# Kernel tuning notes

Measured on AMD Instinct MI355X. Metric: run time of the kernel, lower is better.

The kernel has to match this reference:

```python
import jax, jax.numpy as jnp
import numpy as np

H = 64
VOCAB = 64
SLOTS = 4
N_PASSES = 3
EPS = 1e-5


def _ln(x, g, b):
    m = jnp.mean(x, axis=-1, keepdims=True)
    v = jnp.mean((x - m) ** 2, axis=-1, keepdims=True)
    return (x - m) * jax.lax.rsqrt(v + EPS) * g + b


def setup_inputs() -> dict:
    key = jax.random.key(0)
    ks = iter(jax.random.split(key, 32))
    B, L = 128, 4096
    f = lambda shape, scale=0.05: jax.random.normal(next(ks), shape, dtype=jnp.float32) * scale
    inp = {
        "seq": jax.random.randint(next(ks), (B, L), 0, VOCAB),
        # Encoder
        "embed": f((VOCAB, H), 1.0),
        "ff1_w": f((H, 2 * H)), "ff1_b": jnp.zeros((2 * H,), jnp.float32),
        "ff2_w": f((2 * H, H)), "ff2_b": jnp.zeros((H,), jnp.float32),
        "enc_g": jnp.ones((H,), jnp.float32), "enc_b": jnp.zeros((H,), jnp.float32),
        # ForwardGate
        "g1_w": f((H, H // 2)), "g1_b": jnp.zeros((H // 2,), jnp.float32),
        "g2_w": f((H // 2, 1)), "g2_b": jnp.zeros((1,), jnp.float32),
        # Re-encoding layers (stacked over passes)
        "rq_w": f((N_PASSES, H, H)), "rq_b": jnp.zeros((N_PASSES, H), jnp.float32),
        "rk_w": f((N_PASSES, H, H)), "rk_b": jnp.zeros((N_PASSES, H), jnp.float32),
        "rv_w": f((N_PASSES, H, H)), "rv_b": jnp.zeros((N_PASSES, H), jnp.float32),
        "rn_g": jnp.ones((N_PASSES, H), jnp.float32), "rn_b": jnp.zeros((N_PASSES, H), jnp.float32),
        # ReadHead
        "rd_q_w": f((H, H)), "rd_q_b": jnp.zeros((H,), jnp.float32),
        "out_w": f((H, VOCAB)), "out_b": jnp.zeros((VOCAB,), jnp.float32),
    }
    return inp


def reference(seq, embed, ff1_w, ff1_b, ff2_w, ff2_b, enc_g, enc_b,
              g1_w, g1_b, g2_w, g2_b,
              rq_w, rq_b, rk_w, rk_b, rv_w, rv_b, rn_g, rn_b,
              rd_q_w, rd_q_b, out_w, out_b):
    scale = 1.0 / np.sqrt(H)
    # Encoder: embed + FFN residual + LayerNorm
    h = embed[seq]                                            # (B,L,H)
    ff = jax.nn.relu(h @ ff1_w + ff1_b) @ ff2_w + ff2_b
    hidden = _ln(h + ff, enc_g, enc_b)                        # (B,L,H)
    # Gate scores -> top-k slot selection
    scores = jax.nn.sigmoid(jax.nn.relu(hidden @ g1_w + g1_b) @ g2_w + g2_b)[..., 0]  # (B,L)
    _, idx = jax.lax.top_k(scores, SLOTS)                     # (B,k)
    slots = jnp.take_along_axis(hidden, idx[:, :, None], axis=1)  # (B,k,H)
    # Iterative cross-attention re-encoding
    for p in range(N_PASSES):
        Sq = slots @ rq_w[p] + rq_b[p]                        # (B,k,H)
        Sk = hidden @ rk_w[p] + rk_b[p]                       # (B,L,H)
        Sv = hidden @ rv_w[p] + rv_b[p]
        attn = jax.nn.softmax(jnp.einsum("bkh,blh->bkl", Sq, Sk) * scale, axis=-1)
        slots = _ln(slots + jnp.einsum("bkl,blh->bkh", attn, Sv), rn_g[p], rn_b[p])
    # Read head: attend last-token query over slots
    q = hidden[:, -1, :] @ rd_q_w + rd_q_b                    # (B,H)
    attn = jax.nn.softmax(jnp.einsum("bkh,bh->bk", slots, q) * scale, axis=-1)
    read = jnp.einsum("bk,bkh->bh", attn, slots)
    return read @ out_w + out_b                               # (B,VOCAB)
```

## Files before the change

### kernel.cpp

```cpp
#include <hip/hip_runtime.h>
#include <math.h>

#define H 64
#define VOCAB 64
#define LSEQ 4096
#define NSLOTS 4
#define NP 3
#define EPS 1e-5f

typedef unsigned long long ull;

__device__ __forceinline__ float wsum(float x) {
    #pragma unroll
    for (int m = 1; m < 64; m <<= 1) x += __shfl_xor(x, m);
    return x;
}
__device__ __forceinline__ float wmax(float x) {
    #pragma unroll
    for (int m = 1; m < 64; m <<= 1) x = fmaxf(x, __shfl_xor(x, m));
    return x;
}


__global__ __launch_bounds__(64) void build_all(
    const float* __restrict__ embed,
    const float* __restrict__ ff1_w, const float* __restrict__ ff1_b,
    const float* __restrict__ ff2_w, const float* __restrict__ ff2_b,
    const float* __restrict__ enc_g, const float* __restrict__ enc_b,
    const float* __restrict__ g1_w,  const float* __restrict__ g1_b,
    const float* __restrict__ g2_w,  const float* __restrict__ g2_b,
    const float* __restrict__ rq_w,  const float* __restrict__ rq_b,
    const float* __restrict__ rk_w,  const float* __restrict__ rk_b,
    const float* __restrict__ rv_w,  const float* __restrict__ rv_b,
    const float* __restrict__ rd_q_w, const float* __restrict__ rd_q_b,
    const float* __restrict__ out_w,
    float* __restrict__ enc_t, float* __restrict__ score_t,
    float* __restrict__ c_t, float* __restrict__ q_t,
    float* __restrict__ MT, float* __restrict__ SvT, float* __restrict__ owT)
{
    const int seg  = blockIdx.x >> 6;
    const int v    = blockIdx.x & 63;
    const int lane = threadIdx.x;

    __shared__ float h_s[H];
    __shared__ float a1[2 * H];
    __shared__ float hid_s[H];
    __shared__ float sk_s[H];

    h_s[lane] = embed[v * H + lane];
    __syncthreads();

    float pA[4] = {0, 0, 0, 0}, pB[4] = {0, 0, 0, 0};
    #pragma unroll
    for (int c4 = 0; c4 < 4; c4++)
        #pragma unroll
        for (int d = 0; d < 16; d++) {
            int dd = c4 * 16 + d;
            float hv = h_s[dd];
            pA[c4] += hv * ff1_w[dd * 128 + lane];
            pB[c4] += hv * ff1_w[dd * 128 + lane + 64];
        }
    a1[lane]      = fmaxf(ff1_b[lane]      + ((pA[0] + pA[1]) + (pA[2] + pA[3])), 0.f);
    a1[lane + 64] = fmaxf(ff1_b[lane + 64] + ((pB[0] + pB[1]) + (pB[2] + pB[3])), 0.f);
    __syncthreads();

    float pO[4] = {0, 0, 0, 0};
    #pragma unroll
    for (int c4 = 0; c4 < 4; c4++)
        #pragma unroll
        for (int j = 0; j < 32; j++) {
            int jj = c4 * 32 + j;
            pO[c4] += a1[jj] * ff2_w[jj * H + lane];
        }
    float o = ff2_b[lane] + ((pO[0] + pO[1]) + (pO[2] + pO[3]));

    float x = h_s[lane] + o;
    float s1 = x, s2 = x * x;
    #pragma unroll
    for (int m = 1; m < 64; m <<= 1) { s1 += __shfl_xor(s1, m); s2 += __shfl_xor(s2, m); }
    float mu  = s1 * (1.f / 64.f);
    float var = s2 * (1.f / 64.f) - mu * mu;
    float hid = (x - mu) * rsqrtf(var + EPS) * enc_g[lane] + enc_b[lane];
    hid_s[lane] = hid;
    __syncthreads();

    if (seg == 0) {
        enc_t[v * H + lane] = hid;
        float p = 0.f;
        if (lane < 32) {
            float a[2] = {0, 0};
            #pragma unroll
            for (int c2 = 0; c2 < 2; c2++)
                #pragma unroll
                for (int d = 0; d < 32; d++) {
                    int dd = c2 * 32 + d;
                    a[c2] += hid_s[dd] * g1_w[dd * 32 + lane];
                }
            p = fmaxf(g1_b[lane] + a[0] + a[1], 0.f) * g2_w[lane];
        }
        p = wsum(p);
        if (lane == 0) score_t[v] = 1.f / (1.f + expf(-(p + g2_b[0])));
        float qa[4] = {0, 0, 0, 0};
        #pragma unroll
        for (int c4 = 0; c4 < 4; c4++)
            #pragma unroll
            for (int d = 0; d < 16; d++) {
                int dd = c4 * 16 + d;
                qa[c4] += hid_s[dd] * rd_q_w[dd * H + lane];
            }
        q_t[v * H + lane] = rd_q_b[lane] + ((qa[0] + qa[1]) + (qa[2] + qa[3]));
    }

    if (seg < 3) {
        const int p = seg;
        float ka[4] = {0, 0, 0, 0};
        #pragma unroll
        for (int c4 = 0; c4 < 4; c4++)
            #pragma unroll
            for (int d = 0; d < 16; d++) {
                int dd = c4 * 16 + d;
                ka[c4] += hid_s[dd] * rk_w[(p * H + dd) * H + lane];
            }
        float skv = rk_b[p * H + lane] + ((ka[0] + ka[1]) + (ka[2] + ka[3]));
        sk_s[lane] = skv;
        float cpart = wsum(rq_b[p * H + lane] * skv);
        if (lane == 0) c_t[p * 64 + v] = cpart;
        __syncthreads();
        const float4* rw4 = (const float4*)(rq_w + (size_t)(p * 64 + lane) * 64);
        const float4* sk4 = (const float4*)sk_s;
        float ma[4] = {0, 0, 0, 0};
        #pragma unroll
        for (int i = 0; i < 16; i++) {
            float4 w4 = rw4[i];
            float4 s4 = sk4[i];
            ma[0] += w4.x * s4.x; ma[1] += w4.y * s4.y;
            ma[2] += w4.z * s4.z; ma[3] += w4.w * s4.w;
        }
        MT[p * 4096 + v * 64 + lane] = ((ma[0] + ma[1]) + (ma[2] + ma[3]));
    } else {
        const int p = seg - 3;
        float va[4] = {0, 0, 0, 0};
        #pragma unroll
        for (int c4 = 0; c4 < 4; c4++)
            #pragma unroll
            for (int d = 0; d < 16; d++) {
                int dd = c4 * 16 + d;
                va[c4] += hid_s[dd] * rv_w[(p * H + dd) * H + lane];
            }
        float svv = rv_b[p * H + lane] + ((va[0] + va[1]) + (va[2] + va[3]));
        SvT[p * 4096 + lane * 64 + v] = svv;
        if (seg == 3) owT[v * 64 + lane] = out_w[lane * 64 + v];
    }
}

#define PASS(P, MCUR, MNXT, LOADNEXT)                                          \
{                                                                              \
    float4 vcur[16];                                                           \
    { const float4* b4 = (const float4*)(SvT + (P) * 4096 + lane * 64);        \
      _Pragma("unroll") for (int i = 0; i < 16; i++) vcur[i] = b4[i]; }        \
    if (LOADNEXT) {                                                            \
      const float4* b4 = (const float4*)(MT + ((P) + 1) * 4096 + lane * 64);   \
      _Pragma("unroll") for (int i = 0; i < 16; i++) MNXT[i] = b4[i]; }        \
    sls[wid][lane] = s;                                                        \
    const float4* sp = (const float4*)sls[wid];                                \
    float a0 = 0, a1 = 0, a2 = 0, a3 = 0;                                      \
    _Pragma("unroll") for (int i = 0; i < 16; i++) {                           \
        float4 s4v = sp[i];                                                    \
        a0 += s4v.x * MCUR[i].x; a1 += s4v.y * MCUR[i].y;                      \
        a2 += s4v.z * MCUR[i].z; a3 += s4v.w * MCUR[i].w; }                    \
    float lg = (cc[P] + ((a0 + a1) + (a2 + a3))) * 0.125f;                     \
    float w  = cntf * __expf(lg);                                              \
    float denom = wsum(w);                                                     \
    wls[wid][lane] = w;                                                        \
    const float4* wp = (const float4*)wls[wid];                                \
    float b0 = 0, b1 = 0, b2 = 0, b3 = 0;                                      \
    _Pragma("unroll") for (int i = 0; i < 16; i++) {                           \
        float4 w4 = wp[i];                                                     \
        b0 += w4.x * vcur[i].x; b1 += w4.y * vcur[i].y;                        \
        b2 += w4.z * vcur[i].z; b3 += w4.w * vcur[i].w; }                      \
    float x = s + ((b0 + b1) + (b2 + b3)) / denom;                             \
    float s1 = x, s2v = x * x;                                                 \
    _Pragma("unroll") for (int m = 1; m < 64; m <<= 1) {                       \
        s1 += __shfl_xor(s1, m); s2v += __shfl_xor(s2v, m); }                  \
    float mu  = s1 * (1.f / 64.f);                                             \
    float var = s2v * (1.f / 64.f) - mu * mu;                                  \
    s = (x - mu) * rsqrtf(var + EPS) * rg[P] + rb[P];                          \
}

__global__ __launch_bounds__(256) void run_batches(
    const int*   __restrict__ seq,
    const float* __restrict__ score_t, const float* __restrict__ enc_t,
    const float* __restrict__ c_t, const float* __restrict__ q_t,
    const float* __restrict__ MT, const float* __restrict__ SvT,
    const float* __restrict__ owT,
    const float* __restrict__ rn_g, const float* __restrict__ rn_b,
    const float* __restrict__ out_b,
    float* __restrict__ out)
{
    __shared__ int   whist[4][64];
    __shared__ int   last_sh;
    __shared__ float sls[NSLOTS][64];
    __shared__ float wls[NSLOTS][64];
    __shared__ float slN[NSLOTS][64];
    __shared__ float l4[NSLOTS];
    __shared__ float rbuf[64];

    const int b = blockIdx.x, tid = threadIdx.x;
    const int wid = tid >> 6, lane = tid & 63;

    float sc = score_t[lane];
    float cc[NP], rg[NP], rb[NP];
    #pragma unroll
    for (int p = 0; p < NP; p++) {
        cc[p] = c_t[p * 64 + lane];
        rg[p] = rn_g[p * 64 + lane];
        rb[p] = rn_b[p * 64 + lane];
    }
    float4 mA[16], mB[16];
    {
        const float4* b4 = (const float4*)(MT + lane * 64);
        #pragma unroll
        for (int i = 0; i < 16; i++) mA[i] = b4[i];
    }

    const int4* s4 = (const int4*)(seq + (size_t)b * LSEQ);
    int4 t0 = s4[tid];
    int4 t1 = s4[tid + 256];
    int4 t2 = s4[tid + 512];
    int4 t3 = s4[tid + 768];
    if (tid == 255) last_sh = t3.w;

    whist[wid][lane] = 0;
    {
        int* hw = whist[wid];
        atomicAdd(&hw[t0.x], 1); atomicAdd(&hw[t0.y], 1);
        atomicAdd(&hw[t0.z], 1); atomicAdd(&hw[t0.w], 1);
        atomicAdd(&hw[t1.x], 1); atomicAdd(&hw[t1.y], 1);
        atomicAdd(&hw[t1.z], 1); atomicAdd(&hw[t1.w], 1);
        atomicAdd(&hw[t2.x], 1); atomicAdd(&hw[t2.y], 1);
        atomicAdd(&hw[t2.z], 1); atomicAdd(&hw[t2.w], 1);
        atomicAdd(&hw[t3.x], 1); atomicAdd(&hw[t3.y], 1);
        atomicAdd(&hw[t3.z], 1); atomicAdd(&hw[t3.w], 1);
    }
    __syncthreads();

    const int cnt = whist[0][lane] + whist[1][lane] + whist[2][lane] + whist[3][lane];
    const float cntf = (float)cnt;

    int my_tok = 0;
    {
        float key = cnt > 0 ? sc : -1.f;
        int filled = 0;
        bool have = false;
        #pragma unroll 1
        for (int r = 0; r < NSLOTS && filled < NSLOTS; r++) {
            float m = wmax(key);
            ull win = __ballot(key == m);
            int tk = __ffsll(win) - 1;
            int c  = __shfl(cnt, tk);
            if (!have && (unsigned)(wid - filled) < (unsigned)c) { my_tok = tk; have = true; }
            filled += c;
            if (lane == tk) key = -1.f;
        }
    }

    float s = enc_t[my_tok * 64 + lane];
    float q = q_t[last_sh * 64 + lane];

    PASS(0, mA, mB, 1)
    PASS(1, mB, mA, 1)
    PASS(2, mA, mB, 0)

    float lk = wsum(s * q) * 0.125f;
    if (lane == 0) l4[wid] = lk;
    slN[wid][lane] = s;

    float4 ow[16];
    float ob = 0.f;
    if (wid == 0) {
        const float4* b4 = (const float4*)(owT + lane * 64);
        #pragma unroll
        for (int i = 0; i < 16; i++) ow[i] = b4[i];
        ob = out_b[lane];
    }
    __syncthreads();

    if (wid == 0) {
        float e0 = __expf(l4[0]), e1 = __expf(l4[1]);
        float e2 = __expf(l4[2]), e3 = __expf(l4[3]);
        float dn = e0 + e1 + e2 + e3;
        float r = (e0 * slN[0][lane] + e1 * slN[1][lane]
                 + e2 * slN[2][lane] + e3 * slN[3][lane]) / dn;
        rbuf[lane] = r;
        const float4* rp = (const float4*)rbuf;
        float o0 = 0, o1 = 0, o2 = 0, o3 = 0;
        #pragma unroll
        for (int i = 0; i < 16; i++) {
            float4 rv = rp[i];
            o0 += rv.x * ow[i].x; o1 += rv.y * ow[i].y;
            o2 += rv.z * ow[i].z; o3 += rv.w * ow[i].w;
        }
        out[(size_t)b * VOCAB + lane] = ob + ((o0 + o1) + (o2 + o3));
    }
}

extern "C" void kernel_launch(void* const* d_in, const int* in_sizes, int n_in,
                              void* d_out, int out_size, void* d_ws, size_t ws_size,
                              hipStream_t stream) {
    const int*   seq    = (const int*)  d_in[0];
    const float* embed  = (const float*)d_in[1];
    const float* ff1_w  = (const float*)d_in[2];
    const float* ff1_b  = (const float*)d_in[3];
    const float* ff2_w  = (const float*)d_in[4];
    const float* ff2_b  = (const float*)d_in[5];
    const float* enc_g  = (const float*)d_in[6];
    const float* enc_b  = (const float*)d_in[7];
    const float* g1_w   = (const float*)d_in[8];
    const float* g1_b   = (const float*)d_in[9];
    const float* g2_w   = (const float*)d_in[10];
    const float* g2_b   = (const float*)d_in[11];
    const float* rq_w   = (const float*)d_in[12];
    const float* rq_b   = (const float*)d_in[13];
    const float* rk_w   = (const float*)d_in[14];
    const float* rk_b   = (const float*)d_in[15];
    const float* rv_w   = (const float*)d_in[16];
    const float* rv_b   = (const float*)d_in[17];
    const float* rn_g   = (const float*)d_in[18];
    const float* rn_b   = (const float*)d_in[19];
    const float* rd_q_w = (const float*)d_in[20];
    const float* rd_q_b = (const float*)d_in[21];
    const float* out_w  = (const float*)d_in[22];
    const float* out_b  = (const float*)d_in[23];
    float* out = (float*)d_out;

    const int B = in_sizes[0] / LSEQ;

    float* ws      = (float*)d_ws;
    float* enc_t   = ws;
    float* score_t = ws + 4096;
    float* c_t     = ws + 4160;
    float* q_t     = ws + 4352;
    float* MT      = ws + 8448;
    float* SvT     = ws + 20736;
    float* owT     = ws + 33024;

    build_all<<<384, 64, 0, stream>>>(
        embed, ff1_w, ff1_b, ff2_w, ff2_b, enc_g, enc_b,
        g1_w, g1_b, g2_w, g2_b,
        rq_w, rq_b, rk_w, rk_b, rv_w, rv_b,
        rd_q_w, rd_q_b, out_w,
        enc_t, score_t, c_t, q_t, MT, SvT, owT);

    run_batches<<<B, 256, 0, stream>>>(
        seq, score_t, enc_t, c_t, q_t, MT, SvT, owT,
        rn_g, rn_b, out_b, out);
}
```

Baseline: 27.11 us.

## Fuse table build and batch kernels with a grid-wide atomic barrier

Merges the weight-table build kernel into the per-batch kernel. Each wave of the 128 blocks builds table entries, then all blocks meet at a global atomic-counter barrier before running the attention passes. This removes one kernel launch and overlaps the sequence load and histogram with table building. It adds a memset launch, relies on all blocks being co-resident for the spin barrier, and preloads Sv rows for the next pass alongside M.

Measured after the change: 60.08 us. 2.22x slower.

```diff
diff --git a/kernel.cpp b/kernel.cpp
--- a/kernel.cpp
+++ b/kernel.cpp
@@ -7,6 +7,7 @@
 #define NSLOTS 4
 #define NP 3
 #define EPS 1e-5f
+#define BARRIER_OFF (1u << 20)
 
 typedef unsigned long long ull;
 
@@ -22,7 +23,42 @@
 }
 
 
-__global__ __launch_bounds__(64) void build_all(
+#define PASS(P, MC, MN, VC, VN, CCV, RGV, RBV, LOADNEXT)                       \
+{                                                                              \
+    if (LOADNEXT) {                                                            \
+      const float4* b4 = (const float4*)(MT + ((P) + 1) * 4096 + lane * 64);   \
+      _Pragma("unroll") for (int i = 0; i < 16; i++) MN[i] = b4[i];            \
+      const float4* c4 = (const float4*)(SvT + ((P) + 1) * 4096 + lane * 64);  \
+      _Pragma("unroll") for (int i = 0; i < 16; i++) VN[i] = c4[i];            \
+    }                                                                          \
+    sls[wid][lane] = s;                                                        \
+    const float4* sp = (const float4*)sls[wid];                                \
+    float a0 = 0, a1x = 0, a2 = 0, a3 = 0;                                     \
+    _Pragma("unroll") for (int i = 0; i < 16; i++) {                           \
+        float4 s4v = sp[i];                                                    \
+        a0 += s4v.x * MC[i].x; a1x += s4v.y * MC[i].y;                         \
+        a2 += s4v.z * MC[i].z; a3 += s4v.w * MC[i].w; }                        \
+    float lg = (CCV + ((a0 + a1x) + (a2 + a3))) * 0.125f;                      \
+    float w  = cntf * __expf(lg);                                              \
+    float denom = wsum(w);                                                     \
+    wls[wid][lane] = w;                                                        \
+    const float4* wp = (const float4*)wls[wid];                                \
+    float b0 = 0, b1 = 0, b2 = 0, b3 = 0;                                      \
+    _Pragma("unroll") for (int i = 0; i < 16; i++) {                           \
+        float4 w4 = wp[i];                                                     \
+        b0 += w4.x * VC[i].x; b1 += w4.y * VC[i].y;                            \
+        b2 += w4.z * VC[i].z; b3 += w4.w * VC[i].w; }                          \
+    float x = s + ((b0 + b1) + (b2 + b3)) / denom;                             \
+    float s1 = x, s2v = x * x;                                                 \
+    _Pragma("unroll") for (int m = 1; m < 64; m <<= 1) {                       \
+        s1 += __shfl_xor(s1, m); s2v += __shfl_xor(s2v, m); }                  \
+    float mu  = s1 * (1.f / 64.f);                                             \
+    float var = s2v * (1.f / 64.f) - mu * mu;                                  \
+    s = (x - mu) * rsqrtf(var + EPS) * RGV + RBV;                              \
+}
+
+__global__ __launch_bounds__(256) void fused(
+    const int*   __restrict__ seq,
     const float* __restrict__ embed,
     const float* __restrict__ ff1_w, const float* __restrict__ ff1_b,
     const float* __restrict__ ff2_w, const float* __restrict__ ff2_b,
@@ -32,205 +68,149 @@
     const float* __restrict__ rq_w,  const float* __restrict__ rq_b,
     const float* __restrict__ rk_w,  const float* __restrict__ rk_b,
     const float* __restrict__ rv_w,  const float* __restrict__ rv_b,
+    const float* __restrict__ rn_g,  const float* __restrict__ rn_b,
     const float* __restrict__ rd_q_w, const float* __restrict__ rd_q_b,
-    const float* __restrict__ out_w,
+    const float* __restrict__ out_w, const float* __restrict__ out_b,
     float* __restrict__ enc_t, float* __restrict__ score_t,
     float* __restrict__ c_t, float* __restrict__ q_t,
-    float* __restrict__ MT, float* __restrict__ SvT, float* __restrict__ owT)
-{
-    const int seg  = blockIdx.x >> 6;
-    const int v    = blockIdx.x & 63;
-    const int lane = threadIdx.x;
-
-    __shared__ float h_s[H];
-    __shared__ float a1[2 * H];
-    __shared__ float hid_s[H];
-    __shared__ float sk_s[H];
-
-    h_s[lane] = embed[v * H + lane];
-    __syncthreads();
-
-    float pA[4] = {0, 0, 0, 0}, pB[4] = {0, 0, 0, 0};
-    #pragma unroll
-    for (int c4 = 0; c4 < 4; c4++)
-        #pragma unroll
-        for (int d = 0; d < 16; d++) {
-            int dd = c4 * 16 + d;
-            float hv = h_s[dd];
-            pA[c4] += hv * ff1_w[dd * 128 + lane];
-            pB[c4] += hv * ff1_w[dd * 128 + lane + 64];
-        }
-    a1[lane]      = fmaxf(ff1_b[lane]      + ((pA[0] + pA[1]) + (pA[2] + pA[3])), 0.f);
-    a1[lane + 64] = fmaxf(ff1_b[lane + 64] + ((pB[0] + pB[1]) + (pB[2] + pB[3])), 0.f);
-    __syncthreads();
-
-    float pO[4] = {0, 0, 0, 0};
-    #pragma unroll
-    for (int c4 = 0; c4 < 4; c4++)
-        #pragma unroll
-        for (int j = 0; j < 32; j++) {
-            int jj = c4 * 32 + j;
-            pO[c4] += a1[jj] * ff2_w[jj * H + lane];
-        }
-    float o = ff2_b[lane] + ((pO[0] + pO[1]) + (pO[2] + pO[3]));
-
-    float x = h_s[lane] + o;
-    float s1 = x, s2 = x * x;
-    #pragma unroll
-    for (int m = 1; m < 64; m <<= 1) { s1 += __shfl_xor(s1, m); s2 += __shfl_xor(s2, m); }
-    float mu  = s1 * (1.f / 64.f);
-    float var = s2 * (1.f / 64.f) - mu * mu;
-    float hid = (x - mu) * rsqrtf(var + EPS) * enc_g[lane] + enc_b[lane];
-    hid_s[lane] = hid;
-    __syncthreads();
-
-    if (seg == 0) {
-        enc_t[v * H + lane] = hid;
-        float p = 0.f;
-        if (lane < 32) {
-            float a[2] = {0, 0};
-            #pragma unroll
-            for (int c2 = 0; c2 < 2; c2++)
-                #pragma unroll
-                for (int d = 0; d < 32; d++) {
-                    int dd = c2 * 32 + d;
-                    a[c2] += hid_s[dd] * g1_w[dd * 32 + lane];
-                }
-            p = fmaxf(g1_b[lane] + a[0] + a[1], 0.f) * g2_w[lane];
-        }
-        p = wsum(p);
-        if (lane == 0) score_t[v] = 1.f / (1.f + expf(-(p + g2_b[0])));
-        float qa[4] = {0, 0, 0, 0};
-        #pragma unroll
-        for (int c4 = 0; c4 < 4; c4++)
-            #pragma unroll
-            for (int d = 0; d < 16; d++) {
-                int dd = c4 * 16 + d;
-                qa[c4] += hid_s[dd] * rd_q_w[dd * H + lane];
-            }
-        q_t[v * H + lane] = rd_q_b[lane] + ((qa[0] + qa[1]) + (qa[2] + qa[3]));
-    }
-
-    if (seg < 3) {
-        const int p = seg;
-        float ka[4] = {0, 0, 0, 0};
-        #pragma unroll
-        for (int c4 = 0; c4 < 4; c4++)
-            #pragma unroll
-            for (int d = 0; d < 16; d++) {
-                int dd = c4 * 16 + d;
-                ka[c4] += hid_s[dd] * rk_w[(p * H + dd) * H + lane];
-            }
-        float skv = rk_b[p * H + lane] + ((ka[0] + ka[1]) + (ka[2] + ka[3]));
-        sk_s[lane] = skv;
-        float cpart = wsum(rq_b[p * H + lane] * skv);
-        if (lane == 0) c_t[p * 64 + v] = cpart;
-        __syncthreads();
-        const float4* rw4 = (const float4*)(rq_w + (size_t)(p * 64 + lane) * 64);
-        const float4* sk4 = (const float4*)sk_s;
-        float ma[4] = {0, 0, 0, 0};
-        #pragma unroll
-        for (int i = 0; i < 16; i++) {
-            float4 w4 = rw4[i];
-            float4 s4 = sk4[i];
-            ma[0] += w4.x * s4.x; ma[1] += w4.y * s4.y;
-            ma[2] += w4.z * s4.z; ma[3] += w4.w * s4.w;
-        }
-        MT[p * 4096 + v * 64 + lane] = ((ma[0] + ma[1]) + (ma[2] + ma[3]));
-    } else {
-        const int p = seg - 3;
-        float va[4] = {0, 0, 0, 0};
-        #pragma unroll
-        for (int c4 = 0; c4 < 4; c4++)
-            #pragma unroll
-            for (int d = 0; d < 16; d++) {
-                int dd = c4 * 16 + d;
-                va[c4] += hid_s[dd] * rv_w[(p * H + dd) * H + lane];
-            }
-        float svv = rv_b[p * H + lane] + ((va[0] + va[1]) + (va[2] + va[3]));
-        SvT[p * 4096 + lane * 64 + v] = svv;
-        if (seg == 3) owT[v * 64 + lane] = out_w[lane * 64 + v];
-    }
-}
-
-#define PASS(P, MCUR, MNXT, LOADNEXT)                                          \
-{                                                                              \
-    float4 vcur[16];                                                           \
-    { const float4* b4 = (const float4*)(SvT + (P) * 4096 + lane * 64);        \
-      _Pragma("unroll") for (int i = 0; i < 16; i++) vcur[i] = b4[i]; }        \
-    if (LOADNEXT) {                                                            \
-      const float4* b4 = (const float4*)(MT + ((P) + 1) * 4096 + lane * 64);   \
-      _Pragma("unroll") for (int i = 0; i < 16; i++) MNXT[i] = b4[i]; }        \
-    sls[wid][lane] = s;                                                        \
-    const float4* sp = (const float4*)sls[wid];                                \
-    float a0 = 0, a1 = 0, a2 = 0, a3 = 0;                                      \
-    _Pragma("unroll") for (int i = 0; i < 16; i++) {                           \
-        float4 s4v = sp[i];                                                    \
-        a0 += s4v.x * MCUR[i].x; a1 += s4v.y * MCUR[i].y;                      \
-        a2 += s4v.z * MCUR[i].z; a3 += s4v.w * MCUR[i].w; }                    \
-    float lg = (cc[P] + ((a0 + a1) + (a2 + a3))) * 0.125f;                     \
-    float w  = cntf * __expf(lg);                                              \
-    float denom = wsum(w);                                                     \
-    wls[wid][lane] = w;                                                        \
-    const float4* wp = (const float4*)wls[wid];                                \
-    float b0 = 0, b1 = 0, b2 = 0, b3 = 0;                                      \
-    _Pragma("unroll") for (int i = 0; i < 16; i++) {                           \
-        float4 w4 = wp[i];                                                     \
-        b0 += w4.x * vcur[i].x; b1 += w4.y * vcur[i].y;                        \
-        b2 += w4.z * vcur[i].z; b3 += w4.w * vcur[i].w; }                      \
-    float x = s + ((b0 + b1) + (b2 + b3)) / denom;                             \
-    float s1 = x, s2v = x * x;                                                 \
-    _Pragma("unroll") for (int m = 1; m < 64; m <<= 1) {                       \
-        s1 += __shfl_xor(s1, m); s2v += __shfl_xor(s2v, m); }                  \
-    float mu  = s1 * (1.f / 64.f);                                             \
-    float var = s2v * (1.f / 64.f) - mu * mu;                                  \
-    s = (x - mu) * rsqrtf(var + EPS) * rg[P] + rb[P];                          \
-}
-
-__global__ __launch_bounds__(256) void run_batches(
-    const int*   __restrict__ seq,
-    const float* __restrict__ score_t, const float* __restrict__ enc_t,
-    const float* __restrict__ c_t, const float* __restrict__ q_t,
-    const float* __restrict__ MT, const float* __restrict__ SvT,
-    const float* __restrict__ owT,
-    const float* __restrict__ rn_g, const float* __restrict__ rn_b,
-    const float* __restrict__ out_b,
+    float* __restrict__ MT, float* __restrict__ SvT, float* __restrict__ owT,
+    unsigned* __restrict__ barp,
     float* __restrict__ out)
 {
+    const int bid = blockIdx.x, tid = threadIdx.x;
+    const int wid = tid >> 6, lane = tid & 63;
+
+    __shared__ float bld[4][320];
     __shared__ int   whist[4][64];
     __shared__ int   last_sh;
-    __shared__ float sls[NSLOTS][64];
-    __shared__ float wls[NSLOTS][64];
-    __shared__ float slN[NSLOTS][64];
-    __shared__ float l4[NSLOTS];
+    __shared__ float sls[4][64], wls[4][64], slN[4][64];
+    __shared__ float l4[4];
     __shared__ float rbuf[64];
 
-    const int b = blockIdx.x, tid = threadIdx.x;
-    const int wid = tid >> 6, lane = tid & 63;
-
-    float sc = score_t[lane];
-    float cc[NP], rg[NP], rb[NP];
-    #pragma unroll
-    for (int p = 0; p < NP; p++) {
-        cc[p] = c_t[p * 64 + lane];
-        rg[p] = rn_g[p * 64 + lane];
-        rb[p] = rn_b[p * 64 + lane];
-    }
-    float4 mA[16], mB[16];
-    {
-        const float4* b4 = (const float4*)(MT + lane * 64);
-        #pragma unroll
-        for (int i = 0; i < 16; i++) mA[i] = b4[i];
-    }
-
-    const int4* s4 = (const int4*)(seq + (size_t)b * LSEQ);
+    const int4* s4 = (const int4*)(seq + (size_t)bid * LSEQ);
     int4 t0 = s4[tid];
     int4 t1 = s4[tid + 256];
     int4 t2 = s4[tid + 512];
     int4 t3 = s4[tid + 768];
     if (tid == 255) last_sh = t3.w;
-
     whist[wid][lane] = 0;
+
+    float rg0 = rn_g[lane], rg1 = rn_g[64 + lane], rg2 = rn_g[128 + lane];
+    float rb0 = rn_b[lane], rb1 = rn_b[64 + lane], rb2 = rn_b[128 + lane];
+    float ob  = out_b[lane];
+
+    for (int t = bid * 4 + wid; t < 6 * 64; t += gridDim.x * 4) {
+        const int seg = t >> 6, v = t & 63;
+        float* h_s   = bld[wid];
+        float* a1p   = bld[wid] + 64;
+        float* hid_s = bld[wid] + 192;
+        float* sk_s  = bld[wid] + 256;
+
+        h_s[lane] = embed[v * H + lane];
+        __builtin_amdgcn_wave_barrier();
+
+        float pA[4] = {0, 0, 0, 0}, pB[4] = {0, 0, 0, 0};
+        #pragma unroll
+        for (int c4 = 0; c4 < 4; c4++)
+            #pragma unroll
+            for (int d = 0; d < 16; d++) {
+                int dd = c4 * 16 + d;
+                float hv = h_s[dd];
+                pA[c4] += hv * ff1_w[dd * 128 + lane];
+                pB[c4] += hv * ff1_w[dd * 128 + lane + 64];
+            }
+        a1p[lane]      = fmaxf(ff1_b[lane]      + ((pA[0] + pA[1]) + (pA[2] + pA[3])), 0.f);
+        a1p[lane + 64] = fmaxf(ff1_b[lane + 64] + ((pB[0] + pB[1]) + (pB[2] + pB[3])), 0.f);
+        __builtin_amdgcn_wave_barrier();
+
+        float pO[4] = {0, 0, 0, 0};
+        #pragma unroll
+        for (int c4 = 0; c4 < 4; c4++)
+            #pragma unroll
+            for (int j = 0; j < 32; j++) {
+                int jj = c4 * 32 + j;
+                pO[c4] += a1p[jj] * ff2_w[jj * H + lane];
+            }
+        float o = ff2_b[lane] + ((pO[0] + pO[1]) + (pO[2] + pO[3]));
+
+        float x = h_s[lane] + o;
+        float s1 = x, s2 = x * x;
+        #pragma unroll
+        for (int m = 1; m < 64; m <<= 1) { s1 += __shfl_xor(s1, m); s2 += __shfl_xor(s2, m); }
+        float mu  = s1 * (1.f / 64.f);
+        float var = s2 * (1.f / 64.f) - mu * mu;
+        float hid = (x - mu) * rsqrtf(var + EPS) * enc_g[lane] + enc_b[lane];
+        hid_s[lane] = hid;
+        __builtin_amdgcn_wave_barrier();
+
+        if (seg == 0) {
+            enc_t[v * H + lane] = hid;
+            float p = 0.f;
+            if (lane < 32) {
+                float a[2] = {0, 0};
+                #pragma unroll
+                for (int c2 = 0; c2 < 2; c2++)
+                    #pragma unroll
+                    for (int d = 0; d < 32; d++) {
+                        int dd = c2 * 32 + d;
+                        a[c2] += hid_s[dd] * g1_w[dd * 32 + lane];
+                    }
+                p = fmaxf(g1_b[lane] + a[0] + a[1], 0.f) * g2_w[lane];
+            }
+            p = wsum(p);
+            if (lane == 0) score_t[v] = 1.f / (1.f + expf(-(p + g2_b[0])));
+            float qa[4] = {0, 0, 0, 0};
+            #pragma unroll
+            for (int c4 = 0; c4 < 4; c4++)
+                #pragma unroll
+                for (int d = 0; d < 16; d++) {
+                    int dd = c4 * 16 + d;
+                    qa[c4] += hid_s[dd] * rd_q_w[dd * H + lane];
+                }
+            q_t[v * H + lane] = rd_q_b[lane] + ((qa[0] + qa[1]) + (qa[2] + qa[3]));
+        }
+        if (seg < 3) {
+            const int p = seg;
+            float ka[4] = {0, 0, 0, 0};
+            #pragma unroll
+            for (int c4 = 0; c4 < 4; c4++)
+                #pragma unroll
+                for (int d = 0; d < 16; d++) {
+                    int dd = c4 * 16 + d;
+                    ka[c4] += hid_s[dd] * rk_w[(p * H + dd) * H + lane];
+                }
+            float skv = rk_b[p * H + lane] + ((ka[0] + ka[1]) + (ka[2] + ka[3]));
+            sk_s[lane] = skv;
+            float cpart = wsum(rq_b[p * H + lane] * skv);
+            if (lane == 0) c_t[p * 64 + v] = cpart;
+            __builtin_amdgcn_wave_barrier();
+            const float4* rw4 = (const float4*)(rq_w + (size_t)(p * 64 + lane) * 64);
+            const float4* sk4 = (const float4*)sk_s;
+            float ma[4] = {0, 0, 0, 0};
+            #pragma unroll
+            for (int i = 0; i < 16; i++) {
+                float4 w4 = rw4[i];
+                float4 s4v = sk4[i];
+                ma[0] += w4.x * s4v.x; ma[1] += w4.y * s4v.y;
+                ma[2] += w4.z * s4v.z; ma[3] += w4.w * s4v.w;
+            }
+            MT[p * 4096 + v * 64 + lane] = ((ma[0] + ma[1]) + (ma[2] + ma[3]));
+        } else {
+            const int p = seg - 3;
+            float va[4] = {0, 0, 0, 0};
+            #pragma unroll
+            for (int c4 = 0; c4 < 4; c4++)
+                #pragma unroll
+                for (int d = 0; d < 16; d++) {
+                    int dd = c4 * 16 + d;
+                    va[c4] += hid_s[dd] * rv_w[(p * H + dd) * H + lane];
+                }
+            float svv = rv_b[p * H + lane] + ((va[0] + va[1]) + (va[2] + va[3]));
+            SvT[p * 4096 + lane * 64 + v] = svv;
+            if (seg == 3) owT[v * 64 + lane] = out_w[lane * 64 + v];
+        }
+    }
+
     {
         int* hw = whist[wid];
         atomicAdd(&hw[t0.x], 1); atomicAdd(&hw[t0.y], 1);
@@ -244,8 +224,29 @@
     }
     __syncthreads();
 
+    if (tid == 0) {
+        __threadfence();
+        atomicAdd(barp, 1u);
+        while (atomicAdd(barp, 0u) < (unsigned)gridDim.x)
+            __builtin_amdgcn_s_sleep(2);
+    }
+    __syncthreads();
+    __threadfence();
+
     const int cnt = whist[0][lane] + whist[1][lane] + whist[2][lane] + whist[3][lane];
     const float cntf = (float)cnt;
+
+    float sc = score_t[lane];
+    float4 mA[16], mB[16], vA[16], vB[16];
+    {
+        const float4* p4 = (const float4*)(MT + lane * 64);
+        #pragma unroll
+        for (int i = 0; i < 16; i++) mA[i] = p4[i];
+        const float4* q4 = (const float4*)(SvT + lane * 64);
+        #pragma unroll
+        for (int i = 0; i < 16; i++) vA[i] = q4[i];
+    }
+    float cc0 = c_t[lane], cc1 = c_t[64 + lane], cc2 = c_t[128 + lane];
 
     int my_tok = 0;
     {
@@ -267,21 +268,19 @@
     float s = enc_t[my_tok * 64 + lane];
     float q = q_t[last_sh * 64 + lane];
 
-    PASS(0, mA, mB, 1)
-    PASS(1, mB, mA, 1)
-    PASS(2, mA, mB, 0)
+    PASS(0, mA, mB, vA, vB, cc0, rg0, rb0, 1)
+    PASS(1, mB, mA, vB, vA, cc1, rg1, rb1, 1)
+    PASS(2, mA, mB, vA, vB, cc2, rg2, rb2, 0)
 
     float lk = wsum(s * q) * 0.125f;
     if (lane == 0) l4[wid] = lk;
     slN[wid][lane] = s;
 
     float4 ow[16];
-    float ob = 0.f;
     if (wid == 0) {
         const float4* b4 = (const float4*)(owT + lane * 64);
         #pragma unroll
         for (int i = 0; i < 16; i++) ow[i] = b4[i];
-        ob = out_b[lane];
     }
     __syncthreads();
 
@@ -292,15 +291,16 @@
         float r = (e0 * slN[0][lane] + e1 * slN[1][lane]
                  + e2 * slN[2][lane] + e3 * slN[3][lane]) / dn;
         rbuf[lane] = r;
+        __builtin_amdgcn_wave_barrier();
         const float4* rp = (const float4*)rbuf;
-        float o0 = 0, o1 = 0, o2 = 0, o3 = 0;
+        float o0 = ob, o1 = 0.f, o2 = 0.f, o3 = 0.f;
         #pragma unroll
         for (int i = 0; i < 16; i++) {
             float4 rv = rp[i];
             o0 += rv.x * ow[i].x; o1 += rv.y * ow[i].y;
             o2 += rv.z * ow[i].z; o3 += rv.w * ow[i].w;
         }
-        out[(size_t)b * VOCAB + lane] = ob + ((o0 + o1) + (o2 + o3));
+        out[(size_t)bid * VOCAB + lane] = ((o0 + o1) + (o2 + o3));
     }
 }
 
@@ -343,15 +343,14 @@
     float* MT      = ws + 8448;
     float* SvT     = ws + 20736;
     float* owT     = ws + 33024;
-
-    build_all<<<384, 64, 0, stream>>>(
-        embed, ff1_w, ff1_b, ff2_w, ff2_b, enc_g, enc_b,
+    unsigned* barp = (unsigned*)((char*)d_ws + BARRIER_OFF);
+
+    hipMemsetAsync(barp, 0, 64, stream);
+
+    fused<<<B, 256, 0, stream>>>(
+        seq, embed, ff1_w, ff1_b, ff2_w, ff2_b, enc_g, enc_b,
         g1_w, g1_b, g2_w, g2_b,
-        rq_w, rq_b, rk_w, rk_b, rv_w, rv_b,
-        rd_q_w, rd_q_b, out_w,
-        enc_t, score_t, c_t, q_t, MT, SvT, owT);
-
-    run_batches<<<B, 256, 0, stream>>>(
-        seq, score_t, enc_t, c_t, q_t, MT, SvT, owT,
-        rn_g, rn_b, out_b, out);
-}
+        rq_w, rq_b, rk_w, rk_b, rv_w, rv_b, rn_g, rn_b,
+        rd_q_w, rd_q_b, out_w, out_b,
+        enc_t, score_t, c_t, q_t, MT, SvT, owT, barp, out);
+}
```

## Add fast path when a single top-scoring token fills all slots

Applied to the files above, without the earlier changes.

When a single vocabulary token has the maximum gate score and occurs at least four times in the sequence, all four slots are identical. That block then runs the three passes on one wave only and skips the read-head softmax, since it reduces to the slot itself. The first-pass logit and the Sv/MT loads are hoisted before the histogram barrier. LayerNorm is rescaled to avoid the division by the softmax denominator, with epsilon scaled to match. This is exact for the general input rather than test-specific, but it adds branch divergence across blocks and register pressure.

Measured after the change: 22.76 us. 16.1% less time.

```diff
diff --git a/kernel.cpp b/kernel.cpp
--- a/kernel.cpp
+++ b/kernel.cpp
@@ -132,9 +132,9 @@
         #pragma unroll
         for (int i = 0; i < 16; i++) {
             float4 w4 = rw4[i];
-            float4 s4 = sk4[i];
-            ma[0] += w4.x * s4.x; ma[1] += w4.y * s4.y;
-            ma[2] += w4.z * s4.z; ma[3] += w4.w * s4.w;
+            float4 s4v = sk4[i];
+            ma[0] += w4.x * s4v.x; ma[1] += w4.y * s4v.y;
+            ma[2] += w4.z * s4v.z; ma[3] += w4.w * s4v.w;
         }
         MT[p * 4096 + v * 64 + lane] = ((ma[0] + ma[1]) + (ma[2] + ma[3]));
     } else {
@@ -153,38 +153,38 @@
     }
 }
 
-#define PASS(P, MCUR, MNXT, LOADNEXT)                                          \
+#define PASS(P, MC, MN, CCV, RGV, RBV, LOADNEXT)                               \
 {                                                                              \
     float4 vcur[16];                                                           \
     { const float4* b4 = (const float4*)(SvT + (P) * 4096 + lane * 64);        \
       _Pragma("unroll") for (int i = 0; i < 16; i++) vcur[i] = b4[i]; }        \
     if (LOADNEXT) {                                                            \
       const float4* b4 = (const float4*)(MT + ((P) + 1) * 4096 + lane * 64);   \
-      _Pragma("unroll") for (int i = 0; i < 16; i++) MNXT[i] = b4[i]; }        \
+      _Pragma("unroll") for (int i = 0; i < 16; i++) MN[i] = b4[i]; }          \
     sls[wid][lane] = s;                                                        \
     const float4* sp = (const float4*)sls[wid];                                \
-    float a0 = 0, a1 = 0, a2 = 0, a3 = 0;                                      \
+    float a0 = 0, a1x = 0, a2 = 0, a3 = 0;                                     \
     _Pragma("unroll") for (int i = 0; i < 16; i++) {                           \
         float4 s4v = sp[i];                                                    \
-        a0 += s4v.x * MCUR[i].x; a1 += s4v.y * MCUR[i].y;                      \
-        a2 += s4v.z * MCUR[i].z; a3 += s4v.w * MCUR[i].w; }                    \
-    float lg = (cc[P] + ((a0 + a1) + (a2 + a3))) * 0.125f;                     \
+        a0 += s4v.x * MC[i].x; a1x += s4v.y * MC[i].y;                         \
+        a2 += s4v.z * MC[i].z; a3 += s4v.w * MC[i].w; }                        \
+    float lg = (CCV + ((a0 + a1x) + (a2 + a3))) * 0.125f;                      \
     float w  = cntf * __expf(lg);                                              \
+    wls[wid][lane] = w;                                                        \
     float denom = wsum(w);                                                     \
-    wls[wid][lane] = w;                                                        \
     const float4* wp = (const float4*)wls[wid];                                \
     float b0 = 0, b1 = 0, b2 = 0, b3 = 0;                                      \
     _Pragma("unroll") for (int i = 0; i < 16; i++) {                           \
         float4 w4 = wp[i];                                                     \
         b0 += w4.x * vcur[i].x; b1 += w4.y * vcur[i].y;                        \
         b2 += w4.z * vcur[i].z; b3 += w4.w * vcur[i].w; }                      \
-    float x = s + ((b0 + b1) + (b2 + b3)) / denom;                             \
-    float s1 = x, s2v = x * x;                                                 \
+    float y = s * denom + ((b0 + b1) + (b2 + b3));                             \
+    float s1 = y, s2v = y * y;                                                 \
     _Pragma("unroll") for (int m = 1; m < 64; m <<= 1) {                       \
         s1 += __shfl_xor(s1, m); s2v += __shfl_xor(s2v, m); }                  \
-    float mu  = s1 * (1.f / 64.f);                                             \
-    float var = s2v * (1.f / 64.f) - mu * mu;                                  \
-    s = (x - mu) * rsqrtf(var + EPS) * rg[P] + rb[P];                          \
+    float muy  = s1 * (1.f / 64.f);                                            \
+    float vary = s2v * (1.f / 64.f) - muy * muy;                               \
+    s = (y - muy) * rsqrtf(vary + EPS * denom * denom) * RGV + RBV;            \
 }
 
 __global__ __launch_bounds__(256) void run_batches(
@@ -198,39 +198,60 @@
     float* __restrict__ out)
 {
     __shared__ int   whist[4][64];
-    __shared__ int   last_sh;
-    __shared__ float sls[NSLOTS][64];
-    __shared__ float wls[NSLOTS][64];
-    __shared__ float slN[NSLOTS][64];
-    __shared__ float l4[NSLOTS];
+    __shared__ float sls[4][64], wls[4][64], slN[4][64];
+    __shared__ float l4[4];
     __shared__ float rbuf[64];
 
-    const int b = blockIdx.x, tid = threadIdx.x;
+    const int bid = blockIdx.x, tid = threadIdx.x;
     const int wid = tid >> 6, lane = tid & 63;
 
-    float sc = score_t[lane];
-    float cc[NP], rg[NP], rb[NP];
-    #pragma unroll
-    for (int p = 0; p < NP; p++) {
-        cc[p] = c_t[p * 64 + lane];
-        rg[p] = rn_g[p * 64 + lane];
-        rb[p] = rn_b[p * 64 + lane];
-    }
-    float4 mA[16], mB[16];
-    {
-        const float4* b4 = (const float4*)(MT + lane * 64);
-        #pragma unroll
-        for (int i = 0; i < 16; i++) mA[i] = b4[i];
-    }
-
-    const int4* s4 = (const int4*)(seq + (size_t)b * LSEQ);
+    const int4* s4 = (const int4*)(seq + (size_t)bid * LSEQ);
     int4 t0 = s4[tid];
     int4 t1 = s4[tid + 256];
     int4 t2 = s4[tid + 512];
     int4 t3 = s4[tid + 768];
-    if (tid == 255) last_sh = t3.w;
+    const int last = seq[(size_t)bid * LSEQ + LSEQ - 1];
 
     whist[wid][lane] = 0;
+
+    float sc  = score_t[lane];
+    float cc0 = c_t[lane],      cc1 = c_t[64 + lane],  cc2 = c_t[128 + lane];
+    float rg0 = rn_g[lane],     rg1 = rn_g[64 + lane], rg2 = rn_g[128 + lane];
+    float rb0 = rn_b[lane],     rb1 = rn_b[64 + lane], rb2 = rn_b[128 + lane];
+    float ob  = out_b[lane];
+
+    float mxs  = wmax(sc);
+    ull   bm   = __ballot(sc == mxs);
+    int   t_star = __ffsll(bm) - 1;
+    int   nmax   = __popcll(bm);
+
+    float s = enc_t[t_star * 64 + lane];
+    float q = q_t[last * 64 + lane];
+
+    float4 mA[16], mB[16], vA[16];
+    {
+        const float4* p4 = (const float4*)(MT + lane * 64);
+        #pragma unroll
+        for (int i = 0; i < 16; i++) mA[i] = p4[i];
+        const float4* q4 = (const float4*)(SvT + lane * 64);
+        #pragma unroll
+        for (int i = 0; i < 16; i++) vA[i] = q4[i];
+    }
+
+    float lg0 = 0.f;
+    if (wid == 0) {
+        sls[0][lane] = s;
+        const float4* sp = (const float4*)sls[0];
+        float a0 = 0, a1x = 0, a2 = 0, a3 = 0;
+        #pragma unroll
+        for (int i = 0; i < 16; i++) {
+            float4 s4v = sp[i];
+            a0 += s4v.x * mA[i].x; a1x += s4v.y * mA[i].y;
+            a2 += s4v.z * mA[i].z; a3 += s4v.w * mA[i].w;
+        }
+        lg0 = (cc0 + ((a0 + a1x) + (a2 + a3))) * 0.125f;
+    }
+
     {
         int* hw = whist[wid];
         atomicAdd(&hw[t0.x], 1); atomicAdd(&hw[t0.y], 1);
@@ -246,6 +267,57 @@
 
     const int cnt = whist[0][lane] + whist[1][lane] + whist[2][lane] + whist[3][lane];
     const float cntf = (float)cnt;
+    const int cnt_ts = __shfl(cnt, t_star);
+    const bool spec = (nmax == 1) && (cnt_ts >= NSLOTS);
+
+    if (spec) {
+        if (wid != 0) return;
+
+        {
+            const float4* b4 = (const float4*)(MT + 4096 + lane * 64);
+            #pragma unroll
+            for (int i = 0; i < 16; i++) mB[i] = b4[i];
+            float w = cntf * __expf(lg0);
+            wls[0][lane] = w;
+            float denom = wsum(w);
+            const float4* wp = (const float4*)wls[0];
+            float b0 = 0, b1 = 0, b2 = 0, b3 = 0;
+            #pragma unroll
+            for (int i = 0; i < 16; i++) {
+                float4 w4 = wp[i];
+                b0 += w4.x * vA[i].x; b1 += w4.y * vA[i].y;
+                b2 += w4.z * vA[i].z; b3 += w4.w * vA[i].w;
+            }
+            float y = s * denom + ((b0 + b1) + (b2 + b3));
+            float s1 = y, s2v = y * y;
+            #pragma unroll
+            for (int m = 1; m < 64; m <<= 1) { s1 += __shfl_xor(s1, m); s2v += __shfl_xor(s2v, m); }
+            float muy  = s1 * (1.f / 64.f);
+            float vary = s2v * (1.f / 64.f) - muy * muy;
+            s = (y - muy) * rsqrtf(vary + EPS * denom * denom) * rg0 + rb0;
+        }
+        PASS(1, mB, mA, cc1, rg1, rb1, 1)
+        PASS(2, mA, mB, cc2, rg2, rb2, 0)
+
+        float4 ow[16];
+        {
+            const float4* b4 = (const float4*)(owT + lane * 64);
+            #pragma unroll
+            for (int i = 0; i < 16; i++) ow[i] = b4[i];
+        }
+        rbuf[lane] = s;
+        __builtin_amdgcn_wave_barrier();
+        const float4* rp = (const float4*)rbuf;
+        float o0 = ob, o1 = 0.f, o2 = 0.f, o3 = 0.f;
+        #pragma unroll
+        for (int i = 0; i < 16; i++) {
+            float4 rv = rp[i];
+            o0 += rv.x * ow[i].x; o1 += rv.y * ow[i].y;
+            o2 += rv.z * ow[i].z; o3 += rv.w * ow[i].w;
+        }
+        out[(size_t)bid * VOCAB + lane] = ((o0 + o1) + (o2 + o3));
+        return;
+    }
 
     int my_tok = 0;
     {
@@ -254,8 +326,8 @@
         bool have = false;
         #pragma unroll 1
         for (int r = 0; r < NSLOTS && filled < NSLOTS; r++) {
-            float m = wmax(key);
-            ull win = __ballot(key == m);
+            float m2 = wmax(key);
+            ull win = __ballot(key == m2);
             int tk = __ffsll(win) - 1;
             int c  = __shfl(cnt, tk);
             if (!have && (unsigned)(wid - filled) < (unsigned)c) { my_tok = tk; have = true; }
@@ -264,24 +336,21 @@
         }
     }
 
-    float s = enc_t[my_tok * 64 + lane];
-    float q = q_t[last_sh * 64 + lane];
-
-    PASS(0, mA, mB, 1)
-    PASS(1, mB, mA, 1)
-    PASS(2, mA, mB, 0)
+    s = enc_t[my_tok * 64 + lane];
+
+    PASS(0, mA, mB, cc0, rg0, rb0, 1)
+    PASS(1, mB, mA, cc1, rg1, rb1, 1)
+    PASS(2, mA, mB, cc2, rg2, rb2, 0)
 
     float lk = wsum(s * q) * 0.125f;
     if (lane == 0) l4[wid] = lk;
     slN[wid][lane] = s;
 
     float4 ow[16];
-    float ob = 0.f;
     if (wid == 0) {
         const float4* b4 = (const float4*)(owT + lane * 64);
         #pragma unroll
         for (int i = 0; i < 16; i++) ow[i] = b4[i];
-        ob = out_b[lane];
     }
     __syncthreads();
 
@@ -292,15 +361,16 @@
         float r = (e0 * slN[0][lane] + e1 * slN[1][lane]
                  + e2 * slN[2][lane] + e3 * slN[3][lane]) / dn;
         rbuf[lane] = r;
+        __builtin_amdgcn_wave_barrier();
         const float4* rp = (const float4*)rbuf;
-        float o0 = 0, o1 = 0, o2 = 0, o3 = 0;
+        float o0 = ob, o1 = 0.f, o2 = 0.f, o3 = 0.f;
         #pragma unroll
         for (int i = 0; i < 16; i++) {
             float4 rv = rp[i];
             o0 += rv.x * ow[i].x; o1 += rv.y * ow[i].y;
             o2 += rv.z * ow[i].z; o3 += rv.w * ow[i].w;
         }
-        out[(size_t)b * VOCAB + lane] = ob + ((o0 + o1) + (o2 + o3));
+        out[(size_t)bid * VOCAB + lane] = ((o0 + o1) + (o2 + o3));
     }
 }
 
```
